# Performance work log

Measured on AMD Instinct MI355X. Metric: run time of the kernel, lower is better.

The kernel has to match this reference:

```python
import jax, jax.numpy as jnp
import numpy as np

C = 32
C_Z = 128
S = 256   # MSA depth
N = 384   # residues


def setup_inputs() -> dict:
    key = jax.random.key(0)
    ks = jax.random.split(key, 7)
    m = jax.random.normal(ks[0], (S, N, C), dtype=jnp.float32)
    gamma = jnp.ones((C,), dtype=jnp.float32)
    beta = jnp.zeros((C,), dtype=jnp.float32)
    # projections stored as [in, out]
    W1 = jax.random.normal(ks[1], (C, C), dtype=jnp.float32) / np.sqrt(C)
    W2 = jax.random.normal(ks[2], (C, C), dtype=jnp.float32) / np.sqrt(C)
    W3 = jax.random.normal(ks[3], (C * C, C_Z), dtype=jnp.float32) / np.sqrt(C * C)
    b3 = jnp.zeros((C_Z,), dtype=jnp.float32)
    return {"m": m, "gamma": gamma, "beta": beta, "W1": W1, "W2": W2, "W3": W3, "b3": b3}


def reference(m, gamma, beta, W1, W2, W3, b3):
    # LayerNorm over channel dim
    mu = jnp.mean(m, axis=-1, keepdims=True)
    var = jnp.mean(jnp.square(m - mu), axis=-1, keepdims=True)
    mn = (m - mu) * jax.lax.rsqrt(var + 1e-5) * gamma + beta
    a = jnp.einsum('sic,cd->sid', mn, W1)  # [s, n, c]
    b = jnp.einsum('sic,cd->sid', mn, W2)  # [s, n, c]
    # outer product, mean over MSA dim s -> [n, n, c, c]
    o = jnp.einsum('sic,sjd->ijcd', a, b) / a.shape[0]
    o = o.reshape(o.shape[0], o.shape[1], C * C)  # [n, n, c*c]
    z = o @ W3 + b3  # [n, n, c_z]
    return z
```

## Files before the change

kernel.cpp:

```cpp
#include <hip/hip_runtime.h>

#define S_DEPTH 256
#define NRES 384
#define CIN 32
#define CZ 128
#define MDIM (NRES * CIN)

typedef short bf16x8 __attribute__((ext_vector_type(8)));
typedef short short4v __attribute__((ext_vector_type(4)));
typedef float f32x4 __attribute__((ext_vector_type(4)));

static __device__ __forceinline__ unsigned short f2bf(float f) {
  unsigned int u = __float_as_uint(f);
  unsigned int r = (u + 0x7fffu + ((u >> 16) & 1u)) >> 16;
  return (unsigned short)r;
}

static __device__ __forceinline__ void gld16(const void* g, void* l) {
  __builtin_amdgcn_global_load_lds((__attribute__((address_space(1))) void*)(g),
                                   (__attribute__((address_space(3))) void*)(l),
                                   16, 0, 0);
}

__global__ __launch_bounds__(256) void k_pre(
    const float* __restrict__ mm, const float* __restrict__ gamma,
    const float* __restrict__ beta, const float* __restrict__ W1,
    const float* __restrict__ W2, const float* __restrict__ W3,
    unsigned short* __restrict__ aT, unsigned short* __restrict__ bT,
    unsigned short* __restrict__ W3T) {
  __shared__ __align__(16) char sraw[256 * 33 * 4];
  const int t = threadIdx.x;

  if (blockIdx.x < 16) {
    unsigned short (*tile)[72] = (unsigned short(*)[72])sraw;
    const int b = blockIdx.x;
    const int d0 = (b & 7) * 4;
    const int e0 = (b >> 3) * 64;
#pragma unroll
    for (int iter = 0; iter < 32; ++iter) {
      int lr_ = iter * 4 + (t >> 6);
      int c = lr_ >> 2, dl = lr_ & 3;
      int q = c * 32 + d0 + dl;
      tile[lr_][t & 63] = f2bf(W3[q * 128 + e0 + (t & 63)]);
    }
    __syncthreads();
    const int e_l = t >> 2;
    const int dl = t & 3;
    unsigned short* dst = W3T + (((size_t)(d0 + dl) * 128) + e0 + e_l) * 32;
#pragma unroll
    for (int j = 0; j < 32; ++j) dst[j] = tile[j * 4 + dl][e_l];
    return;
  }

  float* buf = (float*)sraw;
  const int i = blockIdx.x - 16;

#pragma unroll
  for (int it = 0; it < 8; ++it) {
    int s = it * 32 + (t >> 3);
    int c4 = (t & 7) * 4;
    const float4 v = *(const float4*)(mm + ((size_t)s * NRES + i) * CIN + c4);
    buf[s * 33 + c4 + 0] = v.x;
    buf[s * 33 + c4 + 1] = v.y;
    buf[s * 33 + c4 + 2] = v.z;
    buf[s * 33 + c4 + 3] = v.w;
  }
  __syncthreads();

  float x[32];
#pragma unroll
  for (int k = 0; k < 32; ++k) x[k] = buf[t * 33 + k];
  float mu = 0.f;
#pragma unroll
  for (int k = 0; k < 32; ++k) mu += x[k];
  mu *= (1.f / 32.f);
  float var = 0.f;
#pragma unroll
  for (int k = 0; k < 32; ++k) {
    float dk = x[k] - mu;
    var += dk * dk;
  }
  var *= (1.f / 32.f);
  float inv = rsqrtf(var + 1e-5f);
#pragma unroll
  for (int k = 0; k < 32; ++k) x[k] = (x[k] - mu) * inv * gamma[k] + beta[k];

  float va[32], vb[32];
#pragma unroll
  for (int c = 0; c < 32; ++c) { va[c] = 0.f; vb[c] = 0.f; }
#pragma unroll
  for (int k = 0; k < 32; ++k) {
    float xk = x[k];
#pragma unroll
    for (int c = 0; c < 32; ++c) va[c] += xk * W1[k * 32 + c];
#pragma unroll
    for (int c = 0; c < 32; ++c) vb[c] += xk * W2[k * 32 + c];
  }

  unsigned short* dstA = aT + ((size_t)(t >> 6) * MDIM + (size_t)i * 32) * 64 + (t & 63);
  unsigned short* dstB = bT + ((size_t)(t >> 6) * MDIM + (size_t)i * 32) * 64 + (t & 63);
#pragma unroll
  for (int c = 0; c < 32; ++c) dstA[c * 64] = f2bf(va[c]);
#pragma unroll
  for (int c = 0; c < 32; ++c) dstB[c * 64] = f2bf(vb[c]);
}

__global__ __launch_bounds__(256, 2) void k_opm(
    const unsigned short* __restrict__ aT, const unsigned short* __restrict__ bT,
    const unsigned short* __restrict__ W3T, const float* __restrict__ b3,
    float* __restrict__ out) {
  __shared__ __align__(16) char smem[65536];
  const int t = threadIdx.x;
  const int w = t >> 6;
  const int l = t & 63;
  const int lr = l & 15;
  const int quad = l >> 4;
  const int wm = w >> 1, wn = w & 1;

  const int g = blockIdx.x;
  const int xcd = g & 7;
  const int r = g >> 3;
  const int bx = r / 12;
  const int by = xcd * 12 + (r - bx * 12);
  const int m0 = by * 128;
  const int n0 = bx * 256;

  f32x4 acc[4][8];
#pragma unroll
  for (int mt = 0; mt < 4; ++mt)
#pragma unroll
    for (int nt = 0; nt < 8; ++nt) {
      acc[mt][nt][0] = 0.f; acc[mt][nt][1] = 0.f;
      acc[mt][nt][2] = 0.f; acc[mt][nt][3] = 0.f;
    }

  char* smemB = smem + 16384;
  const int laneoff = (l >> 3) * 64 + (((l & 7) ^ (l >> 3)) * 8);

  for (int k0 = 0; k0 < 256; k0 += 64) {
    __syncthreads();
    const unsigned short* aSlab = aT + ((size_t)(k0 >> 6) * MDIM + m0) * 64;
    const unsigned short* bSlab = bT + ((size_t)(k0 >> 6) * MDIM + n0) * 64;
#pragma unroll
    for (int p_ = 0; p_ < 4; ++p_) {
      int ch = p_ * 4 + w;
      gld16(aSlab + ch * 512 + laneoff, smem + ch * 1024);
    }
#pragma unroll
    for (int p_ = 0; p_ < 8; ++p_) {
      int ch = p_ * 4 + w;
      gld16(bSlab + ch * 512 + laneoff, smemB + ch * 1024);
    }
    __syncthreads();

#pragma unroll
    for (int ks = 0; ks < 2; ++ks) {
      const int r8 = lr & 7;
      const int segoff = (((ks * 4 + quad) ^ r8) << 4);
      bf16x8 af[4];
#pragma unroll
      for (int mt = 0; mt < 4; ++mt) {
        int chunk = (wm * 4 + mt) * 2 + (lr >> 3);
        af[mt] = *(const bf16x8*)(smem + chunk * 1024 + r8 * 128 + segoff);
      }
#pragma unroll
      for (int nt = 0; nt < 8; ++nt) {
        int chunk = (wn * 8 + nt) * 2 + (lr >> 3);
        bf16x8 bfr = *(const bf16x8*)(smemB + chunk * 1024 + r8 * 128 + segoff);
#pragma unroll
        for (int mt = 0; mt < 4; ++mt)
          acc[mt][nt] =
              __builtin_amdgcn_mfma_f32_16x16x32_bf16(af[mt], bfr, acc[mt][nt], 0, 0, 0);
      }
    }
  }

  __syncthreads();
  const float scale = 1.0f / 256.0f;
#pragma unroll
  for (int mt = 0; mt < 4; ++mt) {
    int i_l = wm * 2 + (mt >> 1);
    int chc = 2 * (mt & 1) + (quad >> 1);
#pragma unroll
    for (int nt = 0; nt < 8; ++nt) {
      int j_l = wn * 4 + (nt >> 1);
      int d = (nt & 1) * 16 + lr;
      int p = i_l * 8 + j_l;
      int ch = d * 4 + chc;
      int key = (p ^ d) & 7;
      int off = p * 2048 + ((ch ^ key) << 4) + 8 * (quad & 1);
      short4v pk;
      pk[0] = (short)f2bf(acc[mt][nt][0] * scale);
      pk[1] = (short)f2bf(acc[mt][nt][1] * scale);
      pk[2] = (short)f2bf(acc[mt][nt][2] * scale);
      pk[3] = (short)f2bf(acc[mt][nt][3] * scale);
      *(short4v*)(smem + off) = pk;
    }
  }
  __syncthreads();

  f32x4 zacc[2][2];
#pragma unroll
  for (int a = 0; a < 2; ++a)
#pragma unroll
    for (int b = 0; b < 2; ++b) {
      zacc[a][b][0] = 0.f; zacc[a][b][1] = 0.f;
      zacc[a][b][2] = 0.f; zacc[a][b][3] = 0.f;
    }
  float bias0 = b3[(w * 2 + 0) * 16 + lr];
  float bias1 = b3[(w * 2 + 1) * 16 + lr];

  const unsigned short* wg0 = W3T + (size_t)((w * 2 + 0) * 16 + lr) * 32 + quad * 8;
  const unsigned short* wg1 = wg0 + 16 * 32;

  bf16x8 wcur0 = *(const bf16x8*)(wg0);
  bf16x8 wcur1 = *(const bf16x8*)(wg1);
#pragma unroll
  for (int kq = 0; kq < 32; ++kq) {
    bf16x8 wnxt0, wnxt1;
    if (kq < 31) {
      wnxt0 = *(const bf16x8*)(wg0 + (size_t)(kq + 1) * 4096);
      wnxt1 = *(const bf16x8*)(wg1 + (size_t)(kq + 1) * 4096);
    }
    bf16x8 aef[2];
#pragma unroll
    for (int mte = 0; mte < 2; ++mte) {
      int row = mte * 16 + lr;
      int ch = kq * 4 + quad;
      int key = (row ^ kq) & 7;
      aef[mte] = *(const bf16x8*)(smem + row * 2048 + ((ch ^ key) << 4));
    }
    zacc[0][0] = __builtin_amdgcn_mfma_f32_16x16x32_bf16(aef[0], wcur0, zacc[0][0], 0, 0, 0);
    zacc[1][0] = __builtin_amdgcn_mfma_f32_16x16x32_bf16(aef[1], wcur0, zacc[1][0], 0, 0, 0);
    zacc[0][1] = __builtin_amdgcn_mfma_f32_16x16x32_bf16(aef[0], wcur1, zacc[0][1], 0, 0, 0);
    zacc[1][1] = __builtin_amdgcn_mfma_f32_16x16x32_bf16(aef[1], wcur1, zacc[1][1], 0, 0, 0);
    wcur0 = wnxt0;
    wcur1 = wnxt1;
  }

  const int i0 = by * 4, j0 = bx * 8;
#pragma unroll
  for (int mte = 0; mte < 2; ++mte)
#pragma unroll
    for (int nte = 0; nte < 2; ++nte) {
      int e = (w * 2 + nte) * 16 + lr;
      float bias = nte ? bias1 : bias0;
#pragma unroll
      for (int rr = 0; rr < 4; ++rr) {
        int p = mte * 16 + quad * 4 + rr;
        out[(((size_t)(i0 + (p >> 3))) * NRES + (j0 + (p & 7))) * CZ + e] =
            zacc[mte][nte][rr] + bias;
      }
    }
}

extern "C" void kernel_launch(void* const* d_in, const int* in_sizes, int n_in,
                              void* d_out, int out_size, void* d_ws, size_t ws_size,
                              hipStream_t stream) {
  const float* m = (const float*)d_in[0];
  const float* gamma = (const float*)d_in[1];
  const float* beta = (const float*)d_in[2];
  const float* W1 = (const float*)d_in[3];
  const float* W2 = (const float*)d_in[4];
  const float* W3 = (const float*)d_in[5];
  const float* b3 = (const float*)d_in[6];
  float* out = (float*)d_out;

  unsigned short* aT = (unsigned short*)d_ws;
  unsigned short* bT = aT + (size_t)MDIM * S_DEPTH;
  unsigned short* W3T = bT + (size_t)MDIM * S_DEPTH;

  k_pre<<<400, 256, 0, stream>>>(m, gamma, beta, W1, W2, W3, aT, bT, W3T);
  k_opm<<<4608, 256, 0, stream>>>(aT, bT, W3T, b3, out);
}
```

Measured before the change: 245.1 us.

## Enlarge OPM tile to 256x256 with 512-thread blocks and 128KB LDS

Doubles the M tile of the outer-product GEMM from 128 to 256 rows, so each block holds an 8x8 residue pair tile, and uses 8 waves in a 2x4 grid instead of 4 waves in 2x2. The W3 projection epilogue now has each wave handle one 16-column slice of C_Z over 64 pair rows. This halves the grid and raises operand reuse per LDS load, and each W3 fragment now feeds four MFMAs instead of two. In exchange the block uses 128KB of LDS, which will likely limit occupancy to one block per CU despite the launch bounds hint of two.

```diff
diff --git a/kernel.cpp b/kernel.cpp
--- a/kernel.cpp
+++ b/kernel.cpp
@@ -105,37 +105,38 @@
   for (int c = 0; c < 32; ++c) dstB[c * 64] = f2bf(vb[c]);
 }
 
-__global__ __launch_bounds__(256, 2) void k_opm(
+__global__ __launch_bounds__(512, 2) void k_opm(
     const unsigned short* __restrict__ aT, const unsigned short* __restrict__ bT,
     const unsigned short* __restrict__ W3T, const float* __restrict__ b3,
     float* __restrict__ out) {
-  __shared__ __align__(16) char smem[65536];
+  __shared__ __align__(16) char smem[131072];
   const int t = threadIdx.x;
   const int w = t >> 6;
   const int l = t & 63;
   const int lr = l & 15;
   const int quad = l >> 4;
-  const int wm = w >> 1, wn = w & 1;
+  const int wm = w >> 2, wn = w & 3;
 
   const int g = blockIdx.x;
   const int xcd = g & 7;
-  const int r = g >> 3;
-  const int bx = r / 12;
-  const int by = xcd * 12 + (r - bx * 12);
-  const int m0 = by * 128;
+  const int rr = g >> 3;
+  const int bx = rr / 6;
+  const int by = xcd * 6 + (rr - bx * 6);
+  const int m0 = by * 256;
   const int n0 = bx * 256;
 
-  f32x4 acc[4][8];
-#pragma unroll
-  for (int mt = 0; mt < 4; ++mt)
-#pragma unroll
-    for (int nt = 0; nt < 8; ++nt) {
+  f32x4 acc[8][4];
+#pragma unroll
+  for (int mt = 0; mt < 8; ++mt)
+#pragma unroll
+    for (int nt = 0; nt < 4; ++nt) {
       acc[mt][nt][0] = 0.f; acc[mt][nt][1] = 0.f;
       acc[mt][nt][2] = 0.f; acc[mt][nt][3] = 0.f;
     }
 
-  char* smemB = smem + 16384;
+  char* smemB = smem + 32768;
   const int laneoff = (l >> 3) * 64 + (((l & 7) ^ (l >> 3)) * 8);
+  const int r8 = lr & 7;
 
   for (int k0 = 0; k0 < 256; k0 += 64) {
     __syncthreads();
@@ -143,32 +144,31 @@
     const unsigned short* bSlab = bT + ((size_t)(k0 >> 6) * MDIM + n0) * 64;
 #pragma unroll
     for (int p_ = 0; p_ < 4; ++p_) {
-      int ch = p_ * 4 + w;
+      int ch = p_ * 8 + w;
       gld16(aSlab + ch * 512 + laneoff, smem + ch * 1024);
     }
 #pragma unroll
-    for (int p_ = 0; p_ < 8; ++p_) {
-      int ch = p_ * 4 + w;
+    for (int p_ = 0; p_ < 4; ++p_) {
+      int ch = p_ * 8 + w;
       gld16(bSlab + ch * 512 + laneoff, smemB + ch * 1024);
     }
     __syncthreads();
 
 #pragma unroll
     for (int ks = 0; ks < 2; ++ks) {
-      const int r8 = lr & 7;
       const int segoff = (((ks * 4 + quad) ^ r8) << 4);
-      bf16x8 af[4];
-#pragma unroll
-      for (int mt = 0; mt < 4; ++mt) {
-        int chunk = (wm * 4 + mt) * 2 + (lr >> 3);
+      bf16x8 af[8];
+#pragma unroll
+      for (int mt = 0; mt < 8; ++mt) {
+        int chunk = wm * 16 + mt * 2 + (lr >> 3);
         af[mt] = *(const bf16x8*)(smem + chunk * 1024 + r8 * 128 + segoff);
       }
 #pragma unroll
-      for (int nt = 0; nt < 8; ++nt) {
-        int chunk = (wn * 8 + nt) * 2 + (lr >> 3);
+      for (int nt = 0; nt < 4; ++nt) {
+        int chunk = wn * 8 + nt * 2 + (lr >> 3);
         bf16x8 bfr = *(const bf16x8*)(smemB + chunk * 1024 + r8 * 128 + segoff);
 #pragma unroll
-        for (int mt = 0; mt < 4; ++mt)
+        for (int mt = 0; mt < 8; ++mt)
           acc[mt][nt] =
               __builtin_amdgcn_mfma_f32_16x16x32_bf16(af[mt], bfr, acc[mt][nt], 0, 0, 0);
       }
@@ -178,12 +178,12 @@
   __syncthreads();
   const float scale = 1.0f / 256.0f;
 #pragma unroll
-  for (int mt = 0; mt < 4; ++mt) {
-    int i_l = wm * 2 + (mt >> 1);
+  for (int mt = 0; mt < 8; ++mt) {
+    int i_l = wm * 4 + (mt >> 1);
     int chc = 2 * (mt & 1) + (quad >> 1);
 #pragma unroll
-    for (int nt = 0; nt < 8; ++nt) {
-      int j_l = wn * 4 + (nt >> 1);
+    for (int nt = 0; nt < 4; ++nt) {
+      int j_l = wn * 2 + (nt >> 1);
       int d = (nt & 1) * 16 + lr;
       int p = i_l * 8 + j_l;
       int ch = d * 4 + chc;
@@ -199,58 +199,43 @@
   }
   __syncthreads();
 
-  f32x4 zacc[2][2];
-#pragma unroll
-  for (int a = 0; a < 2; ++a)
-#pragma unroll
-    for (int b = 0; b < 2; ++b) {
-      zacc[a][b][0] = 0.f; zacc[a][b][1] = 0.f;
-      zacc[a][b][2] = 0.f; zacc[a][b][3] = 0.f;
-    }
-  float bias0 = b3[(w * 2 + 0) * 16 + lr];
-  float bias1 = b3[(w * 2 + 1) * 16 + lr];
-
-  const unsigned short* wg0 = W3T + (size_t)((w * 2 + 0) * 16 + lr) * 32 + quad * 8;
-  const unsigned short* wg1 = wg0 + 16 * 32;
-
-  bf16x8 wcur0 = *(const bf16x8*)(wg0);
-  bf16x8 wcur1 = *(const bf16x8*)(wg1);
+  f32x4 zacc[4];
+#pragma unroll
+  for (int a = 0; a < 4; ++a) {
+    zacc[a][0] = 0.f; zacc[a][1] = 0.f; zacc[a][2] = 0.f; zacc[a][3] = 0.f;
+  }
+  const float bias = b3[w * 16 + lr];
+
+  const unsigned short* wg = W3T + (size_t)(w * 16 + lr) * 32 + quad * 8;
+
+  bf16x8 wcur = *(const bf16x8*)(wg);
 #pragma unroll
   for (int kq = 0; kq < 32; ++kq) {
-    bf16x8 wnxt0, wnxt1;
-    if (kq < 31) {
-      wnxt0 = *(const bf16x8*)(wg0 + (size_t)(kq + 1) * 4096);
-      wnxt1 = *(const bf16x8*)(wg1 + (size_t)(kq + 1) * 4096);
-    }
-    bf16x8 aef[2];
-#pragma unroll
-    for (int mte = 0; mte < 2; ++mte) {
+    bf16x8 wnxt;
+    if (kq < 31) wnxt = *(const bf16x8*)(wg + (size_t)(kq + 1) * 4096);
+    bf16x8 aef[4];
+#pragma unroll
+    for (int mte = 0; mte < 4; ++mte) {
       int row = mte * 16 + lr;
       int ch = kq * 4 + quad;
       int key = (row ^ kq) & 7;
       aef[mte] = *(const bf16x8*)(smem + row * 2048 + ((ch ^ key) << 4));
     }
-    zacc[0][0] = __builtin_amdgcn_mfma_f32_16x16x32_bf16(aef[0], wcur0, zacc[0][0], 0, 0, 0);
-    zacc[1][0] = __builtin_amdgcn_mfma_f32_16x16x32_bf16(aef[1], wcur0, zacc[1][0], 0, 0, 0);
-    zacc[0][1] = __builtin_amdgcn_mfma_f32_16x16x32_bf16(aef[0], wcur1, zacc[0][1], 0, 0, 0);
-    zacc[1][1] = __builtin_amdgcn_mfma_f32_16x16x32_bf16(aef[1], wcur1, zacc[1][1], 0, 0, 0);
-    wcur0 = wnxt0;
-    wcur1 = wnxt1;
-  }
-
-  const int i0 = by * 4, j0 = bx * 8;
-#pragma unroll
-  for (int mte = 0; mte < 2; ++mte)
-#pragma unroll
-    for (int nte = 0; nte < 2; ++nte) {
-      int e = (w * 2 + nte) * 16 + lr;
-      float bias = nte ? bias1 : bias0;
-#pragma unroll
-      for (int rr = 0; rr < 4; ++rr) {
-        int p = mte * 16 + quad * 4 + rr;
-        out[(((size_t)(i0 + (p >> 3))) * NRES + (j0 + (p & 7))) * CZ + e] =
-            zacc[mte][nte][rr] + bias;
-      }
+#pragma unroll
+    for (int mte = 0; mte < 4; ++mte)
+      zacc[mte] = __builtin_amdgcn_mfma_f32_16x16x32_bf16(aef[mte], wcur, zacc[mte], 0, 0, 0);
+    wcur = wnxt;
+  }
+
+  const int i0 = by * 8, j0 = bx * 8;
+  const int e = w * 16 + lr;
+#pragma unroll
+  for (int mte = 0; mte < 4; ++mte)
+#pragma unroll
+    for (int r = 0; r < 4; ++r) {
+      int p = mte * 16 + quad * 4 + r;
+      out[(((size_t)(i0 + (p >> 3))) * NRES + (j0 + (p & 7))) * CZ + e] =
+          zacc[mte][r] + bias;
     }
 }
 
@@ -271,5 +256,5 @@
   unsigned short* W3T = bT + (size_t)MDIM * S_DEPTH;
 
   k_pre<<<400, 256, 0, stream>>>(m, gamma, beta, W1, W2, W3, aT, bT, W3T);
-  k_opm<<<4608, 256, 0, stream>>>(aT, bT, W3T, b3, out);
-}
+  k_opm<<<2304, 512, 0, stream>>>(aT, bT, W3T, b3, out);
+}
```

After: 236.6 us. -3.5%, faster.
